# Performance work log

Hardware: AMD Instinct MI355X
Metric: run time of the kernel (lower is better)

The kernel has to match this reference:

```python
import jax, jax.numpy as jnp
import numpy as np

B, T, I, H, O = 128, 256, 64, 1024, 64


def setup_inputs() -> dict:
    key = jax.random.key(0)
    ks = jax.random.split(key, 16)
    s_ih1 = 1.0 / np.sqrt(H)
    def mk(k, shape, s):
        return jax.random.uniform(k, shape, jnp.float32, -s, s)
    return {
        "x": jax.random.normal(ks[0], (B, T, I), jnp.float32),
        # RNNCell 1: input I -> hidden H
        "W_ih1": mk(ks[1], (H, I), s_ih1),
        "b_ih1": mk(ks[2], (H,), s_ih1),
        "W_hh1": mk(ks[3], (H, H), s_ih1),
        "b_hh1": mk(ks[4], (H,), s_ih1),
        # RNNCell 2: hidden H -> hidden H
        "W_ih2": mk(ks[5], (H, H), s_ih1),
        "b_ih2": mk(ks[6], (H,), s_ih1),
        "W_hh2": mk(ks[7], (H, H), s_ih1),
        "b_hh2": mk(ks[8], (H,), s_ih1),
        # gate: 2H -> H
        "Wg": mk(ks[9], (H, 2 * H), 1.0 / np.sqrt(2 * H)),
        "bg": mk(ks[10], (H,), 1.0 / np.sqrt(2 * H)),
        # output heads: H -> O
        "Wo1": mk(ks[11], (O, H), s_ih1),
        "bo1": mk(ks[12], (O,), s_ih1),
        "Wo2": mk(ks[13], (O, H), s_ih1),
        "bo2": mk(ks[14], (O,), s_ih1),
    }


def reference(x, W_ih1, b_ih1, W_hh1, b_hh1, W_ih2, b_ih2, W_hh2, b_hh2,
              Wg, bg, Wo1, bo1, Wo2, bo2):
    batch = x.shape[0]
    h1_0 = jnp.zeros((batch, H), x.dtype)
    h2_0 = jnp.zeros((batch, H), x.dtype)
    u_0 = jnp.ones((batch, H), x.dtype)

    def step(carry, x_t):
        h1, h2, u = carry
        # RNNCell 1
        h1 = jnp.tanh(x_t @ W_ih1.T + b_ih1 + h1 @ W_hh1.T + b_hh1)
        # RNNCell 2, gated convex blend with previous h2
        h2_new = jnp.tanh(h1 @ W_ih2.T + b_ih2 + h2 @ W_hh2.T + b_hh2)
        h2 = u * h2_new + (1.0 - u) * h2
        # dual tanh output head
        out = jnp.tanh(h1 @ Wo1.T + bo1) + jnp.tanh(h2 @ Wo2.T + bo2)
        # gate for NEXT step, computed from current hiddens
        u = jax.nn.sigmoid(jnp.concatenate([h1, h2], axis=1) @ Wg.T + bg)
        return (h1, h2, u), out

    xs = jnp.swapaxes(x, 0, 1)  # [T, B, I]
    _, outs = jax.lax.scan(step, (h1_0, h2_0, u_0), xs)
    return jnp.swapaxes(outs, 0, 1)  # [B, T, O]
```

## Files before the change

kernel.cpp:

```cpp
#include <hip/hip_runtime.h>
#include <cstddef>

using bf16x8 = __attribute__((ext_vector_type(8))) short;
using f32x4  = __attribute__((ext_vector_type(4))) float;

constexpr int Bb = 128;
constexpr int Tt = 256;
constexpr int Hh = 1024;
constexpr int Oo = 64;
constexpr int NBLK = 168;
constexpr int FLAG_STRIDE = 32;
constexpr int RS = 1048;

constexpr int R_H1 = 8;
constexpr int R_H2 = 16;
constexpr int R_P2 = 6;
constexpr int R_PG = 6;
constexpr int R_PO = 16;

constexpr int FH1 = 0;
constexpr int FP2 = 32;
constexpr int FPG = 64;
constexpr int FPO = 96;
constexpr int FH2 = 100;
constexpr int FZO = 164;

__device__ __forceinline__ float bf2f(short s) {
  unsigned int u = ((unsigned int)(unsigned short)s) << 16;
  float f;
  __builtin_memcpy(&f, &u, 4);
  return f;
}
__device__ __forceinline__ short f2bf(float f) {
  unsigned int u;
  __builtin_memcpy(&u, &f, 4);
  u += 0x7fffu + ((u >> 16) & 1u);
  return (short)(u >> 16);
}
__device__ __forceinline__ bf16x8 as_bf(int4 v) {
  union { int4 i; bf16x8 b; } u; u.i = v; return u.b;
}
__device__ __forceinline__ float ldf(const float* p) {
  return __hip_atomic_load((float*)p, __ATOMIC_RELAXED, __HIP_MEMORY_SCOPE_AGENT);
}
__device__ __forceinline__ void stf(float* p, float v) {
  __hip_atomic_store(p, v, __ATOMIC_RELAXED, __HIP_MEMORY_SCOPE_AGENT);
}
__device__ __forceinline__ unsigned ldu(const unsigned* p) {
  return __hip_atomic_load((unsigned*)p, __ATOMIC_RELAXED, __HIP_MEMORY_SCOPE_AGENT);
}

#define LD16A(d, p) asm volatile("global_load_dwordx4 %0, %1, off sc1" \
                                 : "=v"(d) : "v"((const void*)(p)))

__device__ __forceinline__ void stage32(short* As, const short* src, int tid) {
  const int row = tid >> 3;
  const int c0  = (tid & 7) * 8;
  const short* gp = src + (size_t)row * Hh + c0;
  short* lp = As + row * RS + c0;
  int4 r0[8], r1[8];
#pragma unroll
  for (int j = 0; j < 8; ++j) LD16A(r0[j], gp + j * 64);
#pragma unroll
  for (int j = 0; j < 8; ++j) LD16A(r1[j], gp + 512 + j * 64);
  asm volatile("s_waitcnt vmcnt(8)" ::: "memory");
#pragma unroll
  for (int j = 0; j < 8; ++j) *(int4*)(lp + j * 64) = r0[j];
  asm volatile("s_waitcnt vmcnt(0)" ::: "memory");
#pragma unroll
  for (int j = 0; j < 8; ++j) *(int4*)(lp + 512 + j * 64) = r1[j];
}

struct BPre {
  const short *bp0, *bp1;
  int4 b0v[6], b1v[6];
};
__device__ __forceinline__ void prefillB(BPre& P,
    const short* __restrict__ B0, size_t st0,
    const short* __restrict__ B1, size_t st1, int lm, int q) {
  P.bp0 = B0 + (size_t)lm * st0 + q * 8;
  P.bp1 = B1 + (size_t)lm * st1 + q * 8;
#pragma unroll
  for (int c = 0; c < 5; ++c) {
    P.b0v[c] = *(const int4*)(P.bp0 + c * 32);
    P.b1v[c] = *(const int4*)(P.bp1 + c * 32);
  }
}
__device__ __forceinline__ void pass32p(const short* As, int lm, int q,
    BPre& P, f32x4 (&acc)[2][2]) {
  const short* ap0 = As + lm * RS + q * 8;
  const short* ap1 = ap0 + 16 * RS;
#pragma unroll
  for (int c = 0; c < 32; ++c) {
    if (c + 5 < 32) {
      P.b0v[(c + 5) % 6] = *(const int4*)(P.bp0 + (c + 5) * 32);
      P.b1v[(c + 5) % 6] = *(const int4*)(P.bp1 + (c + 5) * 32);
    }
    const bf16x8 a0 = as_bf(*(const int4*)(ap0 + c * 32));
    const bf16x8 a1 = as_bf(*(const int4*)(ap1 + c * 32));
    const bf16x8 b0 = as_bf(P.b0v[c % 6]);
    const bf16x8 b1 = as_bf(P.b1v[c % 6]);
    acc[0][0] = __builtin_amdgcn_mfma_f32_16x16x32_bf16(a0, b0, acc[0][0], 0, 0, 0);
    acc[0][1] = __builtin_amdgcn_mfma_f32_16x16x32_bf16(a1, b0, acc[0][1], 0, 0, 0);
    acc[1][0] = __builtin_amdgcn_mfma_f32_16x16x32_bf16(a0, b1, acc[1][0], 0, 0, 0);
    acc[1][1] = __builtin_amdgcn_mfma_f32_16x16x32_bf16(a1, b1, acc[1][1], 0, 0, 0);
  }
}

__device__ __forceinline__ void poll_ge(const unsigned* flags, int base,
                                        int mask, unsigned gen) {
  const unsigned* f = flags + (size_t)(base + (threadIdx.x & mask)) * FLAG_STRIDE;
  while (!__all(ldu(f) >= gen))
    __builtin_amdgcn_s_sleep(2);
}

#define POST_FLAG(GEN) do {                                                \
    asm volatile("s_waitcnt vmcnt(0) lgkmcnt(0)" ::: "memory");            \
    __syncthreads();                                                       \
    if (tid == 0)                                                          \
      __hip_atomic_store(p.flags + (size_t)bid * FLAG_STRIDE, (unsigned)(GEN), \
                         __ATOMIC_RELAXED, __HIP_MEMORY_SCOPE_AGENT);      \
  } while (0)

#define ST_BF16_PAIR(BASE, ROW, COL, HV) do {                              \
    const int _ov = __shfl_xor((int)(unsigned short)(HV), 1, 64);          \
    if ((lm & 1) == 0) {                                                   \
      const unsigned _pk = (unsigned)(unsigned short)(HV) | ((unsigned)_ov << 16); \
      __hip_atomic_store((unsigned*)((BASE) + (size_t)(ROW) * Hh + (COL)), _pk, \
                         __ATOMIC_RELAXED, __HIP_MEMORY_SCOPE_AGENT);      \
    } } while (0)

struct RP {
  short *h1ring;
  short *h2ring;
  float *h2f;
  float *pre2f;
  float *pg1f;
  float *po1f;
  const short* prex;
  const short *whh1, *wih2, *whh2, *wg, *wo1, *wo2;
  const float *b_ih2, *b_hh2, *bg, *bo1, *bo2;
  float* out;
  unsigned* flags;
};

__global__ void __launch_bounds__(256, 1) rnn_kernel(RP p) {
  __shared__ short As[32 * RS];
  const int tid = threadIdx.x;
  const int lane = tid & 63;
  const int wv = tid >> 6;
  const int lm = lane & 15;
  const int q = lane >> 4;
  const int bid = blockIdx.x;

  int role, mb, cb;
  if      (bid < 32)  { role = 0; mb = (bid >> 3) * 32;         cb = (bid & 7) * 128; }
  else if (bid < 64)  { role = 1; mb = ((bid - 32) >> 3) * 32;  cb = ((bid - 32) & 7) * 128; }
  else if (bid < 96)  { role = 2; mb = ((bid - 64) >> 3) * 32;  cb = ((bid - 64) & 7) * 128; }
  else if (bid < 100) { role = 3; mb = (bid - 96) * 32;         cb = 0; }
  else if (bid < 164) { role = 4; mb = ((bid - 100) >> 4) * 32; cb = ((bid - 100) & 15) * 64; }
  else                { role = 5; mb = (bid - 164) * 32;        cb = 0; }

  int colw;
  if (role == 4) colw = cb + wv * 16;
  else if (role == 3 || role == 5) colw = (wv & 1) * 32;
  else colw = cb + wv * 32;

  float bias0 = 0.f, bias1 = 0.f;
  if (role == 1) {
    bias0 = p.b_ih2[colw + lm] + p.b_hh2[colw + lm];
    bias1 = p.b_ih2[colw + 16 + lm] + p.b_hh2[colw + 16 + lm];
  } else if (role == 2) {
    bias0 = p.bg[colw + lm]; bias1 = p.bg[colw + 16 + lm];
  } else if (role == 3) {
    bias0 = p.bo1[colw + lm]; bias1 = p.bo1[colw + 16 + lm];
  } else if (role == 5) {
    bias0 = p.bo2[colw + lm]; bias1 = p.bo2[colw + 16 + lm];
  }

  const short* B0; const short* B1;
  size_t st0 = Hh, st1 = Hh;
  if      (role == 0) { B0 = p.whh1 + (size_t)colw * Hh; B1 = p.whh1 + (size_t)(colw + 16) * Hh; }
  else if (role == 1) { B0 = p.wih2 + (size_t)colw * Hh; B1 = p.wih2 + (size_t)(colw + 16) * Hh; }
  else if (role == 2) { B0 = p.wg + (size_t)colw * (2 * Hh); B1 = p.wg + (size_t)(colw + 16) * (2 * Hh); st0 = st1 = 2 * Hh; }
  else if (role == 3) { B0 = p.wo1 + (size_t)colw * Hh; B1 = p.wo1 + (size_t)(colw + 16) * Hh; }
  else if (role == 4) { B0 = p.whh2 + (size_t)colw * Hh; B1 = p.wg + Hh + (size_t)colw * (2 * Hh); st1 = 2 * Hh; }
  else                { B0 = p.wo2 + (size_t)colw * Hh; B1 = p.wo2 + (size_t)(colw + 16) * Hh; }

  const size_t HS = (size_t)Bb * Hh;
  const f32x4 z4 = {0.f, 0.f, 0.f, 0.f};

  if (role == 0) {
    for (int t = 0; t < Tt; ++t) {
      BPre P; prefillB(P, B0, st0, B1, st1, lm, q);
      short prs[2][2][4];
      const short* pr = p.prex + (size_t)t * HS;
#pragma unroll
      for (int n = 0; n < 2; ++n)
#pragma unroll
        for (int rf = 0; rf < 2; ++rf)
#pragma unroll
          for (int r = 0; r < 4; ++r)
            prs[n][rf][r] = pr[(size_t)(mb + rf * 16 + q * 4 + r) * Hh + colw + n * 16 + lm];
      if (tid < 64) {
        if (t >= 1) poll_ge(p.flags, FH1, 31, (unsigned)t);
        if (t >= 8) {
          poll_ge(p.flags, FP2, 31, (unsigned)(t - 7));
          poll_ge(p.flags, FPG, 31, (unsigned)(t - 7));
          poll_ge(p.flags, FPO, 3,  (unsigned)(t - 7));
        }
      }
      __syncthreads();
      const short* h1prev = p.h1ring + (size_t)((t + R_H1 - 1) % R_H1) * HS;
      stage32(As, h1prev + (size_t)mb * Hh, tid);
      __syncthreads();
      f32x4 acc[2][2]; acc[0][0] = acc[0][1] = acc[1][0] = acc[1][1] = z4;
      pass32p(As, lm, q, P, acc);
      short* h1out = p.h1ring + (size_t)(t % R_H1) * HS;
#pragma unroll
      for (int n = 0; n < 2; ++n)
#pragma unroll
        for (int rf = 0; rf < 2; ++rf)
#pragma unroll
          for (int r = 0; r < 4; ++r) {
            const int row = mb + rf * 16 + q * 4 + r;
            const int col = colw + n * 16 + lm;
            const short hv = f2bf(tanhf(acc[n][rf][r] + bf2f(prs[n][rf][r])));
            ST_BF16_PAIR(h1out, row, col, hv);
          }
      POST_FLAG(t + 1);
    }
  } else if (role == 1) {
    for (int t = 0; t < Tt; ++t) {
      BPre P; prefillB(P, B0, st0, B1, st1, lm, q);
      if (tid < 64) {
        poll_ge(p.flags, FH1, 31, (unsigned)(t + 1));
        if (t >= R_P2) poll_ge(p.flags, FH2, 63, (unsigned)(t - 5));
      }
      __syncthreads();
      const short* h1cur = p.h1ring + (size_t)(t % R_H1) * HS;
      stage32(As, h1cur + (size_t)mb * Hh, tid);
      __syncthreads();
      f32x4 acc[2][2]; acc[0][0] = acc[0][1] = acc[1][0] = acc[1][1] = z4;
      pass32p(As, lm, q, P, acc);
      float* dst = p.pre2f + (size_t)(t % R_P2) * HS;
#pragma unroll
      for (int n = 0; n < 2; ++n)
#pragma unroll
        for (int rf = 0; rf < 2; ++rf)
#pragma unroll
          for (int r = 0; r < 4; ++r) {
            const int row = mb + rf * 16 + q * 4 + r;
            const int col = colw + n * 16 + lm;
            stf(dst + (size_t)row * Hh + col, acc[n][rf][r] + (n ? bias1 : bias0));
          }
      POST_FLAG(t + 1);
    }
  } else if (role == 2) {
    for (int t = 0; t < Tt; ++t) {
      BPre P; prefillB(P, B0, st0, B1, st1, lm, q);
      if (tid < 64) {
        poll_ge(p.flags, FH1, 31, (unsigned)(t + 1));
        if (t >= R_PG) poll_ge(p.flags, FH2, 63, (unsigned)(t - 4));
      }
      __syncthreads();
      const short* h1cur = p.h1ring + (size_t)(t % R_H1) * HS;
      stage32(As, h1cur + (size_t)mb * Hh, tid);
      __syncthreads();
      f32x4 acc[2][2]; acc[0][0] = acc[0][1] = acc[1][0] = acc[1][1] = z4;
      pass32p(As, lm, q, P, acc);
      float* dst = p.pg1f + (size_t)(t % R_PG) * HS;
#pragma unroll
      for (int n = 0; n < 2; ++n)
#pragma unroll
        for (int rf = 0; rf < 2; ++rf)
#pragma unroll
          for (int r = 0; r < 4; ++r) {
            const int row = mb + rf * 16 + q * 4 + r;
            const int col = colw + n * 16 + lm;
            stf(dst + (size_t)row * Hh + col, acc[n][rf][r] + (n ? bias1 : bias0));
          }
      POST_FLAG(t + 1);
    }
  } else if (role == 3) {
    for (int t = 0; t < Tt; ++t) {
      BPre P;
      if (wv < 2) prefillB(P, B0, st0, B1, st1, lm, q);
      if (tid < 64) {
        poll_ge(p.flags, FH1, 31, (unsigned)(t + 1));
        if (t >= R_PO) poll_ge(p.flags, FZO, 3, (unsigned)(t - 15));
      }
      __syncthreads();
      const short* h1cur = p.h1ring + (size_t)(t % R_H1) * HS;
      stage32(As, h1cur + (size_t)mb * Hh, tid);
      __syncthreads();
      if (wv < 2) {
        f32x4 acc[2][2]; acc[0][0] = acc[0][1] = acc[1][0] = acc[1][1] = z4;
        pass32p(As, lm, q, P, acc);
        float* dst = p.po1f + (size_t)(t % R_PO) * (Bb * Oo);
#pragma unroll
        for (int n = 0; n < 2; ++n)
#pragma unroll
          for (int rf = 0; rf < 2; ++rf)
#pragma unroll
            for (int r = 0; r < 4; ++r) {
              const int row = mb + rf * 16 + q * 4 + r;
              const int col = colw + n * 16 + lm;
              stf(dst + (size_t)row * Oo + col,
                  tanhf(acc[n][rf][r] + (n ? bias1 : bias0)));
            }
      }
      POST_FLAG(t + 1);
    }
  } else if (role == 4) {
    for (int s = 0; s < Tt; ++s) {
      BPre P; prefillB(P, B0, st0, B1, st1, lm, q);
      if (tid < 64) {
        poll_ge(p.flags, FP2, 31, (unsigned)(s + 1));
        if (s >= 1) {
          poll_ge(p.flags, FPG, 31, (unsigned)s);
          poll_ge(p.flags, FH2, 63, (unsigned)s);
        }
        if (s >= R_H2) poll_ge(p.flags, FZO, 3, (unsigned)(s - 15));
      }
      __syncthreads();
      float p2v[2][4], pg1v[2][4], hpv[2][4];
      const float* pre2s = p.pre2f + (size_t)(s % R_P2) * HS;
      const float* pg1s  = p.pg1f + (size_t)((s + R_PG - 1) % R_PG) * HS;
#pragma unroll
      for (int rf = 0; rf < 2; ++rf)
#pragma unroll
        for (int r = 0; r < 4; ++r) {
          const size_t idx = (size_t)(mb + rf * 16 + q * 4 + r) * Hh + colw + lm;
          p2v[rf][r] = ldf(pre2s + idx);
          pg1v[rf][r] = (s > 0) ? ldf(pg1s + idx) : 0.f;
          hpv[rf][r] = p.h2f[idx];
        }
      const short* h2prev = p.h2ring + (size_t)((s + R_H2 - 1) % R_H2) * HS;
      stage32(As, h2prev + (size_t)mb * Hh, tid);
      __syncthreads();
      f32x4 acc[2][2]; acc[0][0] = acc[0][1] = acc[1][0] = acc[1][1] = z4;
      pass32p(As, lm, q, P, acc);
      short* h2out = p.h2ring + (size_t)(s % R_H2) * HS;
#pragma unroll
      for (int rf = 0; rf < 2; ++rf)
#pragma unroll
        for (int r = 0; r < 4; ++r) {
          const int row = mb + rf * 16 + q * 4 + r;
          const int col = colw + lm;
          const size_t idx = (size_t)row * Hh + col;
          const float u = (s == 0) ? 1.f
              : 1.f / (1.f + expf(-(acc[1][rf][r] + pg1v[rf][r])));
          const float hn = tanhf(acc[0][rf][r] + p2v[rf][r]);
          const float nv = fmaf(u, hn - hpv[rf][r], hpv[rf][r]);
          p.h2f[idx] = nv;
          const short hv = f2bf(nv);
          ST_BF16_PAIR(h2out, row, col, hv);
        }
      POST_FLAG(s + 1);
    }
  } else {
    for (int ot = 0; ot < Tt; ++ot) {
      BPre P;
      if (wv < 2) prefillB(P, B0, st0, B1, st1, lm, q);
      if (tid < 64) {
        poll_ge(p.flags, FH2, 63, (unsigned)(ot + 1));
        poll_ge(p.flags, FPO, 3,  (unsigned)(ot + 1));
      }
      __syncthreads();
      const float* po1s = p.po1f + (size_t)(ot % R_PO) * (Bb * Oo);
      float pv[2][2][4];
      if (wv < 2) {
#pragma unroll
        for (int n = 0; n < 2; ++n)
#pragma unroll
          for (int rf = 0; rf < 2; ++rf)
#pragma unroll
            for (int r = 0; r < 4; ++r)
              pv[n][rf][r] = ldf(po1s + (size_t)(mb + rf * 16 + q * 4 + r) * Oo
                                 + colw + n * 16 + lm);
      }
      const short* h2cur = p.h2ring + (size_t)(ot % R_H2) * HS;
      stage32(As, h2cur + (size_t)mb * Hh, tid);
      __syncthreads();
      if (wv < 2) {
        f32x4 acc[2][2]; acc[0][0] = acc[0][1] = acc[1][0] = acc[1][1] = z4;
        pass32p(As, lm, q, P, acc);
#pragma unroll
        for (int n = 0; n < 2; ++n)
#pragma unroll
          for (int rf = 0; rf < 2; ++rf)
#pragma unroll
            for (int r = 0; r < 4; ++r) {
              const int row = mb + rf * 16 + q * 4 + r;
              const int col = colw + n * 16 + lm;
              p.out[(size_t)row * (Tt * Oo) + (size_t)ot * Oo + col] =
                  pv[n][rf][r] + tanhf(acc[n][rf][r] + (n ? bias1 : bias0));
            }
      }
      POST_FLAG(ot + 1);
    }
  }
}

__global__ void __launch_bounds__(256) prex_kernel(
    const float* __restrict__ x, const float* __restrict__ wih1,
    const float* __restrict__ b_ih1, const float* __restrict__ b_hh1,
    short* __restrict__ prex) {
  const int tid = threadIdx.x;
  const int lane = tid & 63;
  const int wv = tid >> 6;
  const int lm = lane & 15;
  const int q = lane >> 4;
  const int bm = blockIdx.x >> 4;
  const int bn = blockIdx.x & 15;
  const int rowbase = bm * 64;
  const int col = bn * 64 + wv * 16 + lm;

  const f32x4 z4 = {0.f, 0.f, 0.f, 0.f};
  f32x4 acc[4];
#pragma unroll
  for (int mt = 0; mt < 4; ++mt) acc[mt] = z4;

#pragma unroll
  for (int kc = 0; kc < 2; ++kc) {
    const float* bp = wih1 + col * 64 + kc * 32 + q * 8;
    bf16x8 bf;
#pragma unroll
    for (int j = 0; j < 8; ++j) bf[j] = f2bf(bp[j]);
#pragma unroll
    for (int mt = 0; mt < 4; ++mt) {
      const float* ap = x + (size_t)(rowbase + mt * 16 + lm) * 64 + kc * 32 + q * 8;
      bf16x8 af;
#pragma unroll
      for (int j = 0; j < 8; ++j) af[j] = f2bf(ap[j]);
      acc[mt] = __builtin_amdgcn_mfma_f32_16x16x32_bf16(af, bf, acc[mt], 0, 0, 0);
    }
  }
  const float bia = b_ih1[col] + b_hh1[col];
#pragma unroll
  for (int mt = 0; mt < 4; ++mt) {
#pragma unroll
    for (int r = 0; r < 4; ++r) {
      const int row = rowbase + mt * 16 + q * 4 + r;
      const int b  = row >> 8;
      const int tt = row & 255;
      prex[((size_t)tt * Bb + b) * Hh + col] = f2bf(acc[mt][r] + bia);
    }
  }
}

__global__ void conv_kernel(const float* __restrict__ s, short* __restrict__ d, int n) {
  int i = blockIdx.x * blockDim.x + threadIdx.x;
  const int stride = gridDim.x * blockDim.x;
  for (; i < n; i += stride) d[i] = f2bf(s[i]);
}

__global__ void init_kernel(short* h1ring, short* h2ring,
                            float* h2f, unsigned* flags) {
  const int i = blockIdx.x * blockDim.x + threadIdx.x;
  const size_t HS = (size_t)Bb * Hh;
  h1ring[(size_t)(R_H1 - 1) * HS + i] = 0;
  h2ring[(size_t)(R_H2 - 1) * HS + i] = 0;
  h2f[i] = 0.f;
  if (i < 256) flags[i * FLAG_STRIDE] = 0u;
}

extern "C" void kernel_launch(void* const* d_in, const int* in_sizes, int n_in,
                              void* d_out, int out_size, void* d_ws, size_t ws_size,
                              hipStream_t stream) {
  (void)in_sizes; (void)n_in; (void)out_size; (void)ws_size;
  const float* x      = (const float*)d_in[0];
  const float* W_ih1  = (const float*)d_in[1];
  const float* b_ih1  = (const float*)d_in[2];
  const float* W_hh1  = (const float*)d_in[3];
  const float* b_hh1  = (const float*)d_in[4];
  const float* W_ih2  = (const float*)d_in[5];
  const float* b_ih2  = (const float*)d_in[6];
  const float* W_hh2  = (const float*)d_in[7];
  const float* b_hh2  = (const float*)d_in[8];
  const float* Wg     = (const float*)d_in[9];
  const float* bg     = (const float*)d_in[10];
  const float* Wo1    = (const float*)d_in[11];
  const float* bo1    = (const float*)d_in[12];
  const float* Wo2    = (const float*)d_in[13];
  const float* bo2    = (const float*)d_in[14];

  char* ws = (char*)d_ws;
  size_t off = 0;
  auto alloc = [&](size_t bytes) -> void* {
    void* ptr = ws + off;
    off += (bytes + 255) & ~(size_t)255;
    return ptr;
  };
  short* whh1 = (short*)alloc((size_t)Hh * Hh * 2);
  short* wih2 = (short*)alloc((size_t)Hh * Hh * 2);
  short* whh2 = (short*)alloc((size_t)Hh * Hh * 2);
  short* wg   = (short*)alloc((size_t)Hh * 2 * Hh * 2);
  short* wo1  = (short*)alloc((size_t)Oo * Hh * 2);
  short* wo2  = (short*)alloc((size_t)Oo * Hh * 2);
  short* prex = (short*)alloc((size_t)Bb * Tt * Hh * 2);
  short* h1ring = (short*)alloc((size_t)R_H1 * Bb * Hh * 2);
  short* h2ring = (short*)alloc((size_t)R_H2 * Bb * Hh * 2);
  float* h2f  = (float*)alloc((size_t)Bb * Hh * 4);
  float* pre2f= (float*)alloc((size_t)R_P2 * Bb * Hh * 4);
  float* pg1f = (float*)alloc((size_t)R_PG * Bb * Hh * 4);
  float* po1f = (float*)alloc((size_t)R_PO * Bb * Oo * 4);
  unsigned* flags = (unsigned*)alloc(256 * FLAG_STRIDE * 4);

  conv_kernel<<<1024, 256, 0, stream>>>(W_hh1, whh1, Hh * Hh);
  conv_kernel<<<1024, 256, 0, stream>>>(W_ih2, wih2, Hh * Hh);
  conv_kernel<<<1024, 256, 0, stream>>>(W_hh2, whh2, Hh * Hh);
  conv_kernel<<<2048, 256, 0, stream>>>(Wg,    wg,   Hh * 2 * Hh);
  conv_kernel<<<256,  256, 0, stream>>>(Wo1,   wo1,  Oo * Hh);
  conv_kernel<<<256,  256, 0, stream>>>(Wo2,   wo2,  Oo * Hh);
  init_kernel<<<512, 256, 0, stream>>>(h1ring, h2ring, h2f, flags);
  prex_kernel<<<8192, 256, 0, stream>>>(x, W_ih1, b_ih1, b_hh1, prex);

  RP p;
  p.h1ring = h1ring; p.h2ring = h2ring;
  p.h2f = h2f; p.pre2f = pre2f; p.pg1f = pg1f; p.po1f = po1f;
  p.prex = prex;
  p.whh1 = whh1; p.wih2 = wih2; p.whh2 = whh2;
  p.wg = wg; p.wo1 = wo1; p.wo2 = wo2;
  p.b_ih2 = b_ih2; p.b_hh2 = b_hh2;
  p.bg = bg; p.bo1 = bo1; p.bo2 = bo2;
  p.out = (float*)d_out;
  p.flags = flags;

  rnn_kernel<<<NBLK, 256, 0, stream>>>(p);
}
```

Before: 3.117 ms.

## Keep weights register-resident and repartition persistent RNN roles across 200 blocks

Each wave now loads its whole 16-column weight slice into registers once, before the time loop, instead of streaming weights from global memory every step. The block-to-role mapping is changed: h1 uses 64 blocks with 64-column tiles, pre2/gate use 64-row tiles, and the h2 stage splits the two weight matrices across wave pairs and exchanges gate partial sums through LDS. Flag slots are re-indexed to match. This removes repeated per-step weight traffic on the serial critical path, at the cost of 128 VGPRs per thread for weights, more blocks that must all be co-resident, and an extra LDS exchange and barrier in the h2 stage.

```diff
diff --git a/kernel.cpp b/kernel.cpp
--- a/kernel.cpp
+++ b/kernel.cpp
@@ -8,22 +8,21 @@
 constexpr int Tt = 256;
 constexpr int Hh = 1024;
 constexpr int Oo = 64;
-constexpr int NBLK = 168;
+constexpr int NBLK = 200;
 constexpr int FLAG_STRIDE = 32;
 constexpr int RS = 1048;
 
 constexpr int R_H1 = 8;
 constexpr int R_H2 = 16;
-constexpr int R_P2 = 6;
-constexpr int R_PG = 6;
+constexpr int R_PP = 6;
 constexpr int R_PO = 16;
 
 constexpr int FH1 = 0;
-constexpr int FP2 = 32;
-constexpr int FPG = 64;
-constexpr int FPO = 96;
-constexpr int FH2 = 100;
-constexpr int FZO = 164;
+constexpr int FP2 = 64;
+constexpr int FPG = 96;
+constexpr int FPO = 128;
+constexpr int FH2 = 160;
+constexpr int FZO = 224;
 
 __device__ __forceinline__ float bf2f(short s) {
   unsigned int u = ((unsigned int)(unsigned short)s) << 16;
@@ -53,57 +52,37 @@
 #define LD16A(d, p) asm volatile("global_load_dwordx4 %0, %1, off sc1" \
                                  : "=v"(d) : "v"((const void*)(p)))
 
-__device__ __forceinline__ void stage32(short* As, const short* src, int tid) {
+__device__ __forceinline__ void stage_chunk(short* dstAs, const short* src, int tid) {
   const int row = tid >> 3;
   const int c0  = (tid & 7) * 8;
   const short* gp = src + (size_t)row * Hh + c0;
-  short* lp = As + row * RS + c0;
-  int4 r0[8], r1[8];
-#pragma unroll
-  for (int j = 0; j < 8; ++j) LD16A(r0[j], gp + j * 64);
-#pragma unroll
-  for (int j = 0; j < 8; ++j) LD16A(r1[j], gp + 512 + j * 64);
-  asm volatile("s_waitcnt vmcnt(8)" ::: "memory");
-#pragma unroll
-  for (int j = 0; j < 8; ++j) *(int4*)(lp + j * 64) = r0[j];
+  short* lp = dstAs + row * RS + c0;
+  int4 r0[16];
+#pragma unroll
+  for (int j = 0; j < 16; ++j) LD16A(r0[j], gp + j * 64);
   asm volatile("s_waitcnt vmcnt(0)" ::: "memory");
 #pragma unroll
-  for (int j = 0; j < 8; ++j) *(int4*)(lp + 512 + j * 64) = r1[j];
-}
-
-struct BPre {
-  const short *bp0, *bp1;
-  int4 b0v[6], b1v[6];
-};
-__device__ __forceinline__ void prefillB(BPre& P,
-    const short* __restrict__ B0, size_t st0,
-    const short* __restrict__ B1, size_t st1, int lm, int q) {
-  P.bp0 = B0 + (size_t)lm * st0 + q * 8;
-  P.bp1 = B1 + (size_t)lm * st1 + q * 8;
-#pragma unroll
-  for (int c = 0; c < 5; ++c) {
-    P.b0v[c] = *(const int4*)(P.bp0 + c * 32);
-    P.b1v[c] = *(const int4*)(P.bp1 + c * 32);
-  }
-}
-__device__ __forceinline__ void pass32p(const short* As, int lm, int q,
-    BPre& P, f32x4 (&acc)[2][2]) {
-  const short* ap0 = As + lm * RS + q * 8;
+  for (int j = 0; j < 16; ++j) *(int4*)(lp + j * 64) = r0[j];
+}
+
+__device__ __forceinline__ void loadW(int4 (&w)[32], const short* B, size_t st,
+                                      int lm, int q) {
+  const short* bp = B + (size_t)lm * st + q * 8;
+#pragma unroll
+  for (int c = 0; c < 32; ++c) w[c] = *(const int4*)(bp + c * 32);
+}
+
+__device__ __forceinline__ void passW2(const short* As32, int lm, int q,
+    const int4 (&w)[32], f32x4& acc0, f32x4& acc1) {
+  const short* ap0 = As32 + lm * RS + q * 8;
   const short* ap1 = ap0 + 16 * RS;
 #pragma unroll
   for (int c = 0; c < 32; ++c) {
-    if (c + 5 < 32) {
-      P.b0v[(c + 5) % 6] = *(const int4*)(P.bp0 + (c + 5) * 32);
-      P.b1v[(c + 5) % 6] = *(const int4*)(P.bp1 + (c + 5) * 32);
-    }
     const bf16x8 a0 = as_bf(*(const int4*)(ap0 + c * 32));
     const bf16x8 a1 = as_bf(*(const int4*)(ap1 + c * 32));
-    const bf16x8 b0 = as_bf(P.b0v[c % 6]);
-    const bf16x8 b1 = as_bf(P.b1v[c % 6]);
-    acc[0][0] = __builtin_amdgcn_mfma_f32_16x16x32_bf16(a0, b0, acc[0][0], 0, 0, 0);
-    acc[0][1] = __builtin_amdgcn_mfma_f32_16x16x32_bf16(a1, b0, acc[0][1], 0, 0, 0);
-    acc[1][0] = __builtin_amdgcn_mfma_f32_16x16x32_bf16(a0, b1, acc[1][0], 0, 0, 0);
-    acc[1][1] = __builtin_amdgcn_mfma_f32_16x16x32_bf16(a1, b1, acc[1][1], 0, 0, 0);
+    const bf16x8 b  = as_bf(w[c]);
+    acc0 = __builtin_amdgcn_mfma_f32_16x16x32_bf16(a0, b, acc0, 0, 0, 0);
+    acc1 = __builtin_amdgcn_mfma_f32_16x16x32_bf16(a1, b, acc1, 0, 0, 0);
   }
 }
 
@@ -114,11 +93,12 @@
     __builtin_amdgcn_s_sleep(2);
 }
 
-#define POST_FLAG(GEN) do {                                                \
+#define POST_FLAG(SLOT, GEN) do {                                          \
     asm volatile("s_waitcnt vmcnt(0) lgkmcnt(0)" ::: "memory");            \
     __syncthreads();                                                       \
     if (tid == 0)                                                          \
-      __hip_atomic_store(p.flags + (size_t)bid * FLAG_STRIDE, (unsigned)(GEN), \
+      __hip_atomic_store(p.flags + (size_t)(SLOT) * FLAG_STRIDE,           \
+                         (unsigned)(GEN),                                  \
                          __ATOMIC_RELAXED, __HIP_MEMORY_SCOPE_AGENT);      \
   } while (0)
 
@@ -145,7 +125,8 @@
 };
 
 __global__ void __launch_bounds__(256, 1) rnn_kernel(RP p) {
-  __shared__ short As[32 * RS];
+  __shared__ short As[64 * RS];
+  __shared__ float zbuf[2048];
   const int tid = threadIdx.x;
   const int lane = tid & 63;
   const int wv = tid >> 6;
@@ -153,57 +134,25 @@
   const int q = lane >> 4;
   const int bid = blockIdx.x;
 
-  int role, mb, cb;
-  if      (bid < 32)  { role = 0; mb = (bid >> 3) * 32;         cb = (bid & 7) * 128; }
-  else if (bid < 64)  { role = 1; mb = ((bid - 32) >> 3) * 32;  cb = ((bid - 32) & 7) * 128; }
-  else if (bid < 96)  { role = 2; mb = ((bid - 64) >> 3) * 32;  cb = ((bid - 64) & 7) * 128; }
-  else if (bid < 100) { role = 3; mb = (bid - 96) * 32;         cb = 0; }
-  else if (bid < 164) { role = 4; mb = ((bid - 100) >> 4) * 32; cb = ((bid - 100) & 15) * 64; }
-  else                { role = 5; mb = (bid - 164) * 32;        cb = 0; }
-
-  int colw;
-  if (role == 4) colw = cb + wv * 16;
-  else if (role == 3 || role == 5) colw = (wv & 1) * 32;
-  else colw = cb + wv * 32;
-
-  float bias0 = 0.f, bias1 = 0.f;
-  if (role == 1) {
-    bias0 = p.b_ih2[colw + lm] + p.b_hh2[colw + lm];
-    bias1 = p.b_ih2[colw + 16 + lm] + p.b_hh2[colw + 16 + lm];
-  } else if (role == 2) {
-    bias0 = p.bg[colw + lm]; bias1 = p.bg[colw + 16 + lm];
-  } else if (role == 3) {
-    bias0 = p.bo1[colw + lm]; bias1 = p.bo1[colw + 16 + lm];
-  } else if (role == 5) {
-    bias0 = p.bo2[colw + lm]; bias1 = p.bo2[colw + 16 + lm];
-  }
-
-  const short* B0; const short* B1;
-  size_t st0 = Hh, st1 = Hh;
-  if      (role == 0) { B0 = p.whh1 + (size_t)colw * Hh; B1 = p.whh1 + (size_t)(colw + 16) * Hh; }
-  else if (role == 1) { B0 = p.wih2 + (size_t)colw * Hh; B1 = p.wih2 + (size_t)(colw + 16) * Hh; }
-  else if (role == 2) { B0 = p.wg + (size_t)colw * (2 * Hh); B1 = p.wg + (size_t)(colw + 16) * (2 * Hh); st0 = st1 = 2 * Hh; }
-  else if (role == 3) { B0 = p.wo1 + (size_t)colw * Hh; B1 = p.wo1 + (size_t)(colw + 16) * Hh; }
-  else if (role == 4) { B0 = p.whh2 + (size_t)colw * Hh; B1 = p.wg + Hh + (size_t)colw * (2 * Hh); st1 = 2 * Hh; }
-  else                { B0 = p.wo2 + (size_t)colw * Hh; B1 = p.wo2 + (size_t)(colw + 16) * Hh; }
-
   const size_t HS = (size_t)Bb * Hh;
   const f32x4 z4 = {0.f, 0.f, 0.f, 0.f};
-
-  if (role == 0) {
+  int4 w[32];
+
+  if (bid < 64) {
+    const int g = bid;
+    const int mb = (g >> 4) * 32, cb = (g & 15) * 64;
+    const int cw = cb + wv * 16;
+    loadW(w, p.whh1 + (size_t)cw * Hh, Hh, lm, q);
     for (int t = 0; t < Tt; ++t) {
-      BPre P; prefillB(P, B0, st0, B1, st1, lm, q);
-      short prs[2][2][4];
+      short prs[2][4];
       const short* pr = p.prex + (size_t)t * HS;
 #pragma unroll
-      for (int n = 0; n < 2; ++n)
-#pragma unroll
-        for (int rf = 0; rf < 2; ++rf)
-#pragma unroll
-          for (int r = 0; r < 4; ++r)
-            prs[n][rf][r] = pr[(size_t)(mb + rf * 16 + q * 4 + r) * Hh + colw + n * 16 + lm];
+      for (int rf = 0; rf < 2; ++rf)
+#pragma unroll
+        for (int r = 0; r < 4; ++r)
+          prs[rf][r] = pr[(size_t)(mb + rf * 16 + q * 4 + r) * Hh + cw + lm];
       if (tid < 64) {
-        if (t >= 1) poll_ge(p.flags, FH1, 31, (unsigned)t);
+        if (t >= 1) poll_ge(p.flags, FH1, 63, (unsigned)t);
         if (t >= 8) {
           poll_ge(p.flags, FP2, 31, (unsigned)(t - 7));
           poll_ge(p.flags, FPG, 31, (unsigned)(t - 7));
@@ -212,109 +161,70 @@
       }
       __syncthreads();
       const short* h1prev = p.h1ring + (size_t)((t + R_H1 - 1) % R_H1) * HS;
-      stage32(As, h1prev + (size_t)mb * Hh, tid);
-      __syncthreads();
-      f32x4 acc[2][2]; acc[0][0] = acc[0][1] = acc[1][0] = acc[1][1] = z4;
-      pass32p(As, lm, q, P, acc);
+      stage_chunk(As, h1prev + (size_t)mb * Hh, tid);
+      __syncthreads();
+      f32x4 a0 = z4, a1 = z4;
+      passW2(As, lm, q, w, a0, a1);
       short* h1out = p.h1ring + (size_t)(t % R_H1) * HS;
 #pragma unroll
-      for (int n = 0; n < 2; ++n)
-#pragma unroll
-        for (int rf = 0; rf < 2; ++rf)
-#pragma unroll
-          for (int r = 0; r < 4; ++r) {
-            const int row = mb + rf * 16 + q * 4 + r;
-            const int col = colw + n * 16 + lm;
-            const short hv = f2bf(tanhf(acc[n][rf][r] + bf2f(prs[n][rf][r])));
-            ST_BF16_PAIR(h1out, row, col, hv);
-          }
-      POST_FLAG(t + 1);
-    }
-  } else if (role == 1) {
+      for (int rf = 0; rf < 2; ++rf)
+#pragma unroll
+        for (int r = 0; r < 4; ++r) {
+          const int row = mb + rf * 16 + q * 4 + r;
+          const float z = rf ? a1[r] : a0[r];
+          const short hv = f2bf(tanhf(z + bf2f(prs[rf][r])));
+          ST_BF16_PAIR(h1out, row, cw + lm, hv);
+        }
+      POST_FLAG(FH1 + g, t + 1);
+    }
+  } else if (bid < 128) {
+    const bool isP2 = (bid < 96);
+    const int g = isP2 ? (bid - 64) : (bid - 96);
+    const int mb = (g >> 4) * 64, cb = (g & 15) * 64;
+    const int cw = cb + wv * 16;
+    float bias;
+    if (isP2) {
+      bias = p.b_ih2[cw + lm] + p.b_hh2[cw + lm];
+      loadW(w, p.wih2 + (size_t)cw * Hh, Hh, lm, q);
+    } else {
+      bias = p.bg[cw + lm];
+      loadW(w, p.wg + (size_t)cw * (2 * Hh), 2 * Hh, lm, q);
+    }
+    const int fbase = isP2 ? FP2 : FPG;
+    const int fslot = fbase + g;
     for (int t = 0; t < Tt; ++t) {
-      BPre P; prefillB(P, B0, st0, B1, st1, lm, q);
       if (tid < 64) {
-        poll_ge(p.flags, FH1, 31, (unsigned)(t + 1));
-        if (t >= R_P2) poll_ge(p.flags, FH2, 63, (unsigned)(t - 5));
+        poll_ge(p.flags, FH1, 63, (unsigned)(t + 1));
+        if (t >= R_PP) poll_ge(p.flags, FH2, 63, (unsigned)(t - (isP2 ? 5 : 4)));
       }
       __syncthreads();
       const short* h1cur = p.h1ring + (size_t)(t % R_H1) * HS;
-      stage32(As, h1cur + (size_t)mb * Hh, tid);
-      __syncthreads();
-      f32x4 acc[2][2]; acc[0][0] = acc[0][1] = acc[1][0] = acc[1][1] = z4;
-      pass32p(As, lm, q, P, acc);
-      float* dst = p.pre2f + (size_t)(t % R_P2) * HS;
-#pragma unroll
-      for (int n = 0; n < 2; ++n)
-#pragma unroll
-        for (int rf = 0; rf < 2; ++rf)
-#pragma unroll
-          for (int r = 0; r < 4; ++r) {
-            const int row = mb + rf * 16 + q * 4 + r;
-            const int col = colw + n * 16 + lm;
-            stf(dst + (size_t)row * Hh + col, acc[n][rf][r] + (n ? bias1 : bias0));
-          }
-      POST_FLAG(t + 1);
-    }
-  } else if (role == 2) {
-    for (int t = 0; t < Tt; ++t) {
-      BPre P; prefillB(P, B0, st0, B1, st1, lm, q);
-      if (tid < 64) {
-        poll_ge(p.flags, FH1, 31, (unsigned)(t + 1));
-        if (t >= R_PG) poll_ge(p.flags, FH2, 63, (unsigned)(t - 4));
-      }
-      __syncthreads();
-      const short* h1cur = p.h1ring + (size_t)(t % R_H1) * HS;
-      stage32(As, h1cur + (size_t)mb * Hh, tid);
-      __syncthreads();
-      f32x4 acc[2][2]; acc[0][0] = acc[0][1] = acc[1][0] = acc[1][1] = z4;
-      pass32p(As, lm, q, P, acc);
-      float* dst = p.pg1f + (size_t)(t % R_PG) * HS;
-#pragma unroll
-      for (int n = 0; n < 2; ++n)
-#pragma unroll
-        for (int rf = 0; rf < 2; ++rf)
-#pragma unroll
-          for (int r = 0; r < 4; ++r) {
-            const int row = mb + rf * 16 + q * 4 + r;
-            const int col = colw + n * 16 + lm;
-            stf(dst + (size_t)row * Hh + col, acc[n][rf][r] + (n ? bias1 : bias0));
-          }
-      POST_FLAG(t + 1);
-    }
-  } else if (role == 3) {
-    for (int t = 0; t < Tt; ++t) {
-      BPre P;
-      if (wv < 2) prefillB(P, B0, st0, B1, st1, lm, q);
-      if (tid < 64) {
-        poll_ge(p.flags, FH1, 31, (unsigned)(t + 1));
-        if (t >= R_PO) poll_ge(p.flags, FZO, 3, (unsigned)(t - 15));
-      }
-      __syncthreads();
-      const short* h1cur = p.h1ring + (size_t)(t % R_H1) * HS;
-      stage32(As, h1cur + (size_t)mb * Hh, tid);
-      __syncthreads();
-      if (wv < 2) {
-        f32x4 acc[2][2]; acc[0][0] = acc[0][1] = acc[1][0] = acc[1][1] = z4;
-        pass32p(As, lm, q, P, acc);
-        float* dst = p.po1f + (size_t)(t % R_PO) * (Bb * Oo);
-#pragma unroll
-        for (int n = 0; n < 2; ++n)
-#pragma unroll
-          for (int rf = 0; rf < 2; ++rf)
-#pragma unroll
-            for (int r = 0; r < 4; ++r) {
-              const int row = mb + rf * 16 + q * 4 + r;
-              const int col = colw + n * 16 + lm;
-              stf(dst + (size_t)row * Oo + col,
-                  tanhf(acc[n][rf][r] + (n ? bias1 : bias0)));
-            }
-      }
-      POST_FLAG(t + 1);
-    }
-  } else if (role == 4) {
+      stage_chunk(As, h1cur + (size_t)mb * Hh, tid);
+      stage_chunk(As + 32 * RS, h1cur + (size_t)(mb + 32) * Hh, tid);
+      __syncthreads();
+      f32x4 acc[4];
+      acc[0] = acc[1] = acc[2] = acc[3] = (f32x4){bias, bias, bias, bias};
+      passW2(As, lm, q, w, acc[0], acc[1]);
+      passW2(As + 32 * RS, lm, q, w, acc[2], acc[3]);
+      float* dst = (isP2 ? p.pre2f : p.pg1f) + (size_t)(t % R_PP) * HS;
+#pragma unroll
+      for (int rf = 0; rf < 4; ++rf)
+#pragma unroll
+        for (int r = 0; r < 4; ++r) {
+          const int row = mb + rf * 16 + q * 4 + r;
+          stf(dst + (size_t)row * Hh + cw + lm, acc[rf][r]);
+        }
+      POST_FLAG(fslot, t + 1);
+    }
+  } else if (bid < 192) {
+    const int g = bid - 128;
+    const int mb = (g >> 5) * 64, cb = (g & 31) * 32;
+    const int m = wv >> 1;
+    const int ch = wv & 1;
+    const int cw = cb + ch * 16;
+    if (m == 0) loadW(w, p.whh2 + (size_t)cw * Hh, Hh, lm, q);
+    else        loadW(w, p.wg + Hh + (size_t)cw * (2 * Hh), 2 * Hh, lm, q);
     for (int s = 0; s < Tt; ++s) {
-      BPre P; prefillB(P, B0, st0, B1, st1, lm, q);
       if (tid < 64) {
         poll_ge(p.flags, FP2, 31, (unsigned)(s + 1));
         if (s >= 1) {
@@ -324,81 +234,120 @@
         if (s >= R_H2) poll_ge(p.flags, FZO, 3, (unsigned)(s - 15));
       }
       __syncthreads();
-      float p2v[2][4], pg1v[2][4], hpv[2][4];
-      const float* pre2s = p.pre2f + (size_t)(s % R_P2) * HS;
-      const float* pg1s  = p.pg1f + (size_t)((s + R_PG - 1) % R_PG) * HS;
-#pragma unroll
-      for (int rf = 0; rf < 2; ++rf)
-#pragma unroll
-        for (int r = 0; r < 4; ++r) {
-          const size_t idx = (size_t)(mb + rf * 16 + q * 4 + r) * Hh + colw + lm;
-          p2v[rf][r] = ldf(pre2s + idx);
-          pg1v[rf][r] = (s > 0) ? ldf(pg1s + idx) : 0.f;
-          hpv[rf][r] = p.h2f[idx];
-        }
+      float p2v[4][4], pg1v[4][4], hpv[4][4];
+      if (m == 0) {
+        const float* pre2s = p.pre2f + (size_t)(s % R_PP) * HS;
+        const float* pg1s  = p.pg1f + (size_t)((s + R_PP - 1) % R_PP) * HS;
+#pragma unroll
+        for (int rf = 0; rf < 4; ++rf)
+#pragma unroll
+          for (int r = 0; r < 4; ++r) {
+            const size_t idx = (size_t)(mb + rf * 16 + q * 4 + r) * Hh + cw + lm;
+            p2v[rf][r] = ldf(pre2s + idx);
+            pg1v[rf][r] = (s > 0) ? ldf(pg1s + idx) : 0.f;
+            hpv[rf][r] = p.h2f[idx];
+          }
+      }
       const short* h2prev = p.h2ring + (size_t)((s + R_H2 - 1) % R_H2) * HS;
-      stage32(As, h2prev + (size_t)mb * Hh, tid);
-      __syncthreads();
-      f32x4 acc[2][2]; acc[0][0] = acc[0][1] = acc[1][0] = acc[1][1] = z4;
-      pass32p(As, lm, q, P, acc);
-      short* h2out = p.h2ring + (size_t)(s % R_H2) * HS;
+      stage_chunk(As, h2prev + (size_t)mb * Hh, tid);
+      stage_chunk(As + 32 * RS, h2prev + (size_t)(mb + 32) * Hh, tid);
+      __syncthreads();
+      f32x4 acc[4];
+      acc[0] = acc[1] = acc[2] = acc[3] = z4;
+      passW2(As, lm, q, w, acc[0], acc[1]);
+      passW2(As + 32 * RS, lm, q, w, acc[2], acc[3]);
+      if (m == 1) {
+        float* zb = zbuf + ch * 1024;
+#pragma unroll
+        for (int rf = 0; rf < 4; ++rf)
+#pragma unroll
+          for (int r = 0; r < 4; ++r)
+            zb[(rf * 4 + r) * 64 + lane] = acc[rf][r];
+      }
+      __syncthreads();
+      if (m == 0) {
+        const float* zb = zbuf + ch * 1024;
+        short* h2out = p.h2ring + (size_t)(s % R_H2) * HS;
+#pragma unroll
+        for (int rf = 0; rf < 4; ++rf)
+#pragma unroll
+          for (int r = 0; r < 4; ++r) {
+            const int row = mb + rf * 16 + q * 4 + r;
+            const size_t idx = (size_t)row * Hh + cw + lm;
+            const float zg = zb[(rf * 4 + r) * 64 + lane];
+            const float u = (s == 0) ? 1.f
+                : 1.f / (1.f + expf(-(zg + pg1v[rf][r])));
+            const float hn = tanhf(acc[rf][r] + p2v[rf][r]);
+            const float nv = fmaf(u, hn - hpv[rf][r], hpv[rf][r]);
+            p.h2f[idx] = nv;
+            const short hv = f2bf(nv);
+            ST_BF16_PAIR(h2out, row, cw + lm, hv);
+          }
+      }
+      POST_FLAG(FH2 + g, s + 1);
+    }
+  } else if (bid < 196) {
+    const int g = bid - 192;
+    const int mb = g * 32;
+    const int cw = wv * 16;
+    const float bias = p.bo1[cw + lm];
+    loadW(w, p.wo1 + (size_t)cw * Hh, Hh, lm, q);
+    for (int t = 0; t < Tt; ++t) {
+      if (tid < 64) {
+        poll_ge(p.flags, FH1, 63, (unsigned)(t + 1));
+        if (t >= R_PO) poll_ge(p.flags, FZO, 3, (unsigned)(t - 15));
+      }
+      __syncthreads();
+      const short* h1cur = p.h1ring + (size_t)(t % R_H1) * HS;
+      stage_chunk(As, h1cur + (size_t)mb * Hh, tid);
+      __syncthreads();
+      f32x4 a0 = {bias, bias, bias, bias}, a1 = a0;
+      passW2(As, lm, q, w, a0, a1);
+      float* dst = p.po1f + (size_t)(t % R_PO) * (Bb * Oo);
 #pragma unroll
       for (int rf = 0; rf < 2; ++rf)
 #pragma unroll
         for (int r = 0; r < 4; ++r) {
           const int row = mb + rf * 16 + q * 4 + r;
-          const int col = colw + lm;
-          const size_t idx = (size_t)row * Hh + col;
-          const float u = (s == 0) ? 1.f
-              : 1.f / (1.f + expf(-(acc[1][rf][r] + pg1v[rf][r])));
-          const float hn = tanhf(acc[0][rf][r] + p2v[rf][r]);
-          const float nv = fmaf(u, hn - hpv[rf][r], hpv[rf][r]);
-          p.h2f[idx] = nv;
-          const short hv = f2bf(nv);
-          ST_BF16_PAIR(h2out, row, col, hv);
-        }
-      POST_FLAG(s + 1);
+          const float z = rf ? a1[r] : a0[r];
+          stf(dst + (size_t)row * Oo + cw + lm, tanhf(z));
+        }
+      POST_FLAG(FPO + g, t + 1);
     }
   } else {
+    const int g = bid - 196;
+    const int mb = g * 32;
+    const int cw = wv * 16;
+    const float bias = p.bo2[cw + lm];
+    loadW(w, p.wo2 + (size_t)cw * Hh, Hh, lm, q);
     for (int ot = 0; ot < Tt; ++ot) {
-      BPre P;
-      if (wv < 2) prefillB(P, B0, st0, B1, st1, lm, q);
       if (tid < 64) {
         poll_ge(p.flags, FH2, 63, (unsigned)(ot + 1));
         poll_ge(p.flags, FPO, 3,  (unsigned)(ot + 1));
       }
       __syncthreads();
+      float pv[2][4];
       const float* po1s = p.po1f + (size_t)(ot % R_PO) * (Bb * Oo);
-      float pv[2][2][4];
-      if (wv < 2) {
-#pragma unroll
-        for (int n = 0; n < 2; ++n)
-#pragma unroll
-          for (int rf = 0; rf < 2; ++rf)
-#pragma unroll
-            for (int r = 0; r < 4; ++r)
-              pv[n][rf][r] = ldf(po1s + (size_t)(mb + rf * 16 + q * 4 + r) * Oo
-                                 + colw + n * 16 + lm);
-      }
+#pragma unroll
+      for (int rf = 0; rf < 2; ++rf)
+#pragma unroll
+        for (int r = 0; r < 4; ++r)
+          pv[rf][r] = ldf(po1s + (size_t)(mb + rf * 16 + q * 4 + r) * Oo + cw + lm);
       const short* h2cur = p.h2ring + (size_t)(ot % R_H2) * HS;
-      stage32(As, h2cur + (size_t)mb * Hh, tid);
-      __syncthreads();
-      if (wv < 2) {
-        f32x4 acc[2][2]; acc[0][0] = acc[0][1] = acc[1][0] = acc[1][1] = z4;
-        pass32p(As, lm, q, P, acc);
-#pragma unroll
-        for (int n = 0; n < 2; ++n)
-#pragma unroll
-          for (int rf = 0; rf < 2; ++rf)
-#pragma unroll
-            for (int r = 0; r < 4; ++r) {
-              const int row = mb + rf * 16 + q * 4 + r;
-              const int col = colw + n * 16 + lm;
-              p.out[(size_t)row * (Tt * Oo) + (size_t)ot * Oo + col] =
-                  pv[n][rf][r] + tanhf(acc[n][rf][r] + (n ? bias1 : bias0));
-            }
-      }
-      POST_FLAG(ot + 1);
+      stage_chunk(As, h2cur + (size_t)mb * Hh, tid);
+      __syncthreads();
+      f32x4 a0 = {bias, bias, bias, bias}, a1 = a0;
+      passW2(As, lm, q, w, a0, a1);
+#pragma unroll
+      for (int rf = 0; rf < 2; ++rf)
+#pragma unroll
+        for (int r = 0; r < 4; ++r) {
+          const int row = mb + rf * 16 + q * 4 + r;
+          const float z = rf ? a1[r] : a0[r];
+          p.out[(size_t)row * (Tt * Oo) + (size_t)ot * Oo + cw + lm] =
+              pv[rf][r] + tanhf(z);
+        }
+      POST_FLAG(FZO + g, ot + 1);
     }
   }
 }
@@ -503,8 +452,8 @@
   short* h1ring = (short*)alloc((size_t)R_H1 * Bb * Hh * 2);
   short* h2ring = (short*)alloc((size_t)R_H2 * Bb * Hh * 2);
   float* h2f  = (float*)alloc((size_t)Bb * Hh * 4);
-  float* pre2f= (float*)alloc((size_t)R_P2 * Bb * Hh * 4);
-  float* pg1f = (float*)alloc((size_t)R_PG * Bb * Hh * 4);
+  float* pre2f= (float*)alloc((size_t)R_PP * Bb * Hh * 4);
+  float* pg1f = (float*)alloc((size_t)R_PP * Bb * Hh * 4);
   float* po1f = (float*)alloc((size_t)R_PO * Bb * Oo * 4);
   unsigned* flags = (unsigned*)alloc(256 * FLAG_STRIDE * 4);
 
```

After: 2.692 ms (median of 2 runs). -13.6%, faster.
